# Performance work log

Hardware: AMD Instinct MI355X
Metric: run time of the kernel (lower is better)

Reference implementation:

```python
import jax, jax.numpy as jnp
import numpy as np

B, S, D, H = 2, 2048, 1024, 16
DK = D // H


def setup_inputs() -> dict:
    key = jax.random.key(0)
    ks = jax.random.split(key, 13)
    scale = 1.0 / np.sqrt(D)
    return {
        "query": jax.random.normal(ks[0], (B, S, D), jnp.float32),
        "key": jax.random.normal(ks[1], (B, S, D), jnp.float32),
        "value": jax.random.normal(ks[2], (B, S, D), jnp.float32),
        "mask": jax.random.randint(ks[3], (B, S, S), 0, 2, jnp.int32),
        "Wq": jax.random.normal(ks[4], (D, D), jnp.float32) * scale,
        "bq": jnp.zeros((D,), jnp.float32),
        "Wk": jax.random.normal(ks[5], (D, D), jnp.float32) * scale,
        "bk": jnp.zeros((D,), jnp.float32),
        "Wv": jax.random.normal(ks[6], (D, D), jnp.float32) * scale,
        "bv": jnp.zeros((D,), jnp.float32),
        "Wo": jax.random.normal(ks[7], (D, D), jnp.float32) * scale,
        "bo": jnp.zeros((D,), jnp.float32),
    }


def _split_heads(x):
    # [B,S,D] -> [B,H,S,DK]
    b, s, _ = x.shape
    return x.reshape(b, s, H, DK).transpose(0, 2, 1, 3)


def reference(query, key, value, mask, Wq, bq, Wk, bk, Wv, bv, Wo, bo):
    q = _split_heads(query @ Wq + bq)
    k = _split_heads(key @ Wk + bk)
    v = _split_heads(value @ Wv + bv)
    # scaled dot-product scores [B,H,Sq,Sk]
    scores = jnp.einsum("bhqd,bhkd->bhqk", q, k) / jnp.sqrt(jnp.float32(DK))
    scores = jnp.where(mask[:, None, :, :] == 0, jnp.float32(-1e9), scores)
    p_attn = jax.nn.softmax(scores, axis=-1)  # dropout p=0.0 -> identity
    x = jnp.einsum("bhqk,bhkd->bhqd", p_attn, v)
    x = x.transpose(0, 2, 1, 3).reshape(query.shape[0], -1, D)
    return x @ Wo + bo
```

## Files before the change

### kernel.cpp

```cpp
#include <hip/hip_runtime.h>
#include <cstdint>

#define B_ 2
#define S_ 2048
#define D_ 1024
#define H_ 16
#define DK_ 64
#define SCALE_ 0.18033688011112042f

typedef float f32x4 __attribute__((ext_vector_type(4)));
typedef float f32x16 __attribute__((ext_vector_type(16)));
typedef __bf16 bf16x8 __attribute__((ext_vector_type(8)));
typedef unsigned short u16x8 __attribute__((ext_vector_type(8)));
typedef unsigned short u16x4 __attribute__((ext_vector_type(4)));
typedef unsigned int u32x4 __attribute__((ext_vector_type(4)));

__device__ __forceinline__ unsigned short f2bf(float x) {
  unsigned int u = __builtin_bit_cast(unsigned int, x);
  u += 0x7FFFu + ((u >> 16) & 1u);
  return (unsigned short)(u >> 16);
}

__device__ __forceinline__ void gload16(const void* g, void* l) {
  __builtin_amdgcn_global_load_lds((__attribute__((address_space(1))) void*)(void*)g,
                                   (__attribute__((address_space(3))) void*)l, 16, 0, 0);
}

__device__ __forceinline__ float exp2v(float x) {
  float r;
  asm("v_exp_f32 %0, %1" : "=v"(r) : "v"(x));
  return r;
}

__device__ __forceinline__ unsigned int cvtpk(float a, float b) {
  unsigned int r;
  asm("v_cvt_pk_bf16_f32 %0, %1, %2" : "=v"(r) : "v"(a), "v"(b));
  return r;
}

__device__ __forceinline__ unsigned int bit_mask(unsigned int w, int bit) {
#if __has_builtin(__builtin_amdgcn_sbfe)
  return (unsigned int)__builtin_amdgcn_sbfe((int)w, bit, 1);
#else
  return (unsigned int)((int)(w << (31 - bit)) >> 31);
#endif
}

__global__ __launch_bounds__(256) void prep_kernel(
    const float* __restrict__ q, const float* __restrict__ k, const float* __restrict__ v,
    unsigned short* __restrict__ oq, unsigned short* __restrict__ ok,
    unsigned short* __restrict__ ov,
    const float* __restrict__ w0, const float* __restrict__ w1,
    const float* __restrict__ w2, const float* __restrict__ w3,
    unsigned short* o0, unsigned short* o1, unsigned short* o2, unsigned short* o3,
    const int* __restrict__ mask, unsigned int* __restrict__ mb) {
  __shared__ float t[32][33];
  const int bid = blockIdx.x;
  const int tid = threadIdx.x;
  if (bid < 6144) {
    const int z = bid >> 11, vb = bid & 2047;
    const float* in = z == 0 ? q : z == 1 ? k : v;
    unsigned short* out = z == 0 ? oq : z == 1 ? ok : ov;
    const int n = B_ * S_ * D_;
    int idx = vb * 256 + tid;
#pragma unroll
    for (int i = idx * 4; i < n; i += 2048 * 256 * 4) {
      f32x4 vv = *(const f32x4*)(in + i);
      u16x4 o;
#pragma unroll
      for (int j = 0; j < 4; ++j) o[j] = f2bf(vv[j]);
      *(u16x4*)(out + i) = o;
    }
  } else if (bid < 10240) {
    const int r = bid - 6144;
    const int z = r >> 10, rr = r & 1023;
    const float* W;
    unsigned short* O;
    float sc = 1.f;
    if (z == 0) { W = w0; O = o0; sc = SCALE_; }
    else if (z == 1) { W = w1; O = o1; }
    else if (z == 2) { W = w2; O = o2; }
    else { W = w3; O = o3; }
    const int n0 = (rr & 31) * 32, k0 = (rr >> 5) * 32;
    const int tx = tid & 31, ty = tid >> 5;
    for (int i = ty; i < 32; i += 8) t[i][tx] = W[(size_t)(k0 + i) * D_ + n0 + tx];
    __syncthreads();
    for (int i = ty; i < 32; i += 8) O[(size_t)(n0 + i) * D_ + k0 + tx] = f2bf(t[tx][i] * sc);
  } else {
    const int wid = ((bid - 10240) << 2) + (tid >> 6);
    const int lane = tid & 63;
    size_t base = (size_t)wid << 6;
    unsigned long long bits = __ballot(mask[base + lane] != 0);
    if (lane == 0) *(unsigned long long*)(mb + (base >> 5)) = bits;
  }
}

template <int MODE, int TN, int NWN>
__device__ __forceinline__ void gemm_t(const unsigned short* __restrict__ A,
                                       const unsigned short* __restrict__ BT,
                                       const float* __restrict__ bias, float bsc,
                                       void* __restrict__ Cp, int M, int N, int K) {
  constexpr int NWM = 4 / NWN;
  constexpr int WM = 128 / NWM;
  constexpr int WN = TN / NWN;
  constexpr int MR = WM / 16, NR = WN / 16;
  __shared__ unsigned short Al[2][128 * 32];
  __shared__ unsigned short Bl[2][TN * 32];
  const int tid = threadIdx.x;
  const int lane = tid & 63;
  const int w = tid >> 6;
  const int wr = w / NWN, wc = w % NWN;
  const int nwg = gridDim.x * gridDim.y;
  const int wg = blockIdx.x + gridDim.x * blockIdx.y;
  const int work = (wg & 7) * (nwg >> 3) + (wg >> 3);
  const int nx = N / TN;
  const int m0 = (work / nx) * 128, n0 = (work % nx) * TN;

  f32x4 acc[MR][NR] = {};
  const int nk = K / 32;
  const int srow = lane >> 2;
  const int scol = ((lane & 3) ^ ((lane >> 3) & 3)) * 8;

  const int fr = lane & 15;
  const int rsw = ((lane >> 4) ^ ((fr >> 1) & 3)) * 8;

  auto stage = [&](int kt, int bufi) {
#pragma unroll
    for (int it = 0; it < 2; ++it) {
      int chunk = it * 4 + w;
      gload16(A + (size_t)(m0 + chunk * 16 + srow) * K + kt * 32 + scol,
              &Al[bufi][chunk * 512]);
    }
#pragma unroll
    for (int it = 0; it < TN / 64; ++it) {
      int chunk = it * 4 + w;
      gload16(BT + (size_t)(n0 + chunk * 16 + srow) * K + kt * 32 + scol,
              &Bl[bufi][chunk * 512]);
    }
  };

  stage(0, 0);
  for (int kt = 0; kt < nk; ++kt) {
    const int buf = kt & 1;
    __syncthreads();
    if (kt + 1 < nk) stage(kt + 1, buf ^ 1);
    bf16x8 af[MR], bf[NR];
#pragma unroll
    for (int i = 0; i < MR; ++i)
      af[i] = __builtin_bit_cast(bf16x8,
          *(const u16x8*)&Al[buf][(wr * WM + i * 16 + fr) * 32 + rsw]);
#pragma unroll
    for (int j = 0; j < NR; ++j)
      bf[j] = __builtin_bit_cast(bf16x8,
          *(const u16x8*)&Bl[buf][(wc * WN + j * 16 + fr) * 32 + rsw]);
    __builtin_amdgcn_s_setprio(1);
#pragma unroll
    for (int i = 0; i < MR; ++i)
#pragma unroll
      for (int j = 0; j < NR; ++j)
        acc[i][j] = __builtin_amdgcn_mfma_f32_16x16x32_bf16(af[i], bf[j], acc[i][j], 0, 0, 0);
    __builtin_amdgcn_s_setprio(0);
  }

  const int rg = (lane >> 4) * 4;
  const int cg = lane & 15;
#pragma unroll
  for (int i = 0; i < MR; ++i)
#pragma unroll
    for (int j = 0; j < NR; ++j) {
      int col = n0 + wc * WN + j * 16 + cg;
      float bv = bias[col] * bsc;
#pragma unroll
      for (int e = 0; e < 4; ++e) {
        int row = m0 + wr * WM + i * 16 + rg + e;
        float v = acc[i][j][e] + bv;
        if (MODE == 1)
          ((float*)Cp)[(size_t)row * N + col] = v;
        else if (MODE == 0)
          ((unsigned short*)Cp)[(size_t)row * N + col] = f2bf(v);
        else
          ((unsigned short*)Cp)[((size_t)(row >> 11) * D_ + col) * S_ + (row & (S_ - 1))] = f2bf(v);
      }
    }
}

__global__ __launch_bounds__(256) void qkv_gemm_kernel(
    const unsigned short* __restrict__ xq, const unsigned short* __restrict__ xk,
    const unsigned short* __restrict__ xv, const unsigned short* __restrict__ wtq,
    const unsigned short* __restrict__ wtk, const unsigned short* __restrict__ wtv,
    const float* __restrict__ bq, const float* __restrict__ bk, const float* __restrict__ bv,
    unsigned short* q, unsigned short* k, unsigned short* vt) {
  if (blockIdx.z == 0)
    gemm_t<0, 128, 2>(xq, wtq, bq, SCALE_, (void*)q, B_ * S_, D_, D_);
  else if (blockIdx.z == 1)
    gemm_t<0, 128, 2>(xk, wtk, bk, 1.f, (void*)k, B_ * S_, D_, D_);
  else
    gemm_t<2, 128, 2>(xv, wtv, bv, 1.f, (void*)vt, B_ * S_, D_, D_);
}

__global__ __launch_bounds__(256) void out_gemm_kernel(const unsigned short* __restrict__ x,
                                                       const unsigned short* __restrict__ wto,
                                                       const float* __restrict__ bo,
                                                       float* __restrict__ out) {
  gemm_t<1, 64, 1>(x, wto, bo, 1.f, (void*)out, B_ * S_, D_, D_);
}

__global__ __launch_bounds__(256, 2) void attn_kernel(const unsigned short* __restrict__ Q,
                                                      const unsigned short* __restrict__ K,
                                                      const unsigned short* __restrict__ Vt,
                                                      const unsigned int* __restrict__ mb,
                                                      unsigned short* __restrict__ X) {
  __shared__ unsigned short Kl[2][128 * 64];
  __shared__ unsigned short Vl[2][2][64 * 64];

  const int tid = threadIdx.x;
  const int lane = tid & 63;
  const int w = tid >> 6;
  const int ql = lane & 31;
  const int hi = lane >> 5;

  const int wg = blockIdx.x + gridDim.x * blockIdx.y;
  const int swz = (wg & 7) * 64 + (wg >> 3);
  const int qt = swz & 15;
  const int bh = swz >> 4;
  const int b = bh >> 4, h = bh & 15;
  const int q_g = qt * 128 + w * 32 + ql;

  const size_t qkbase = ((size_t)b * S_) * D_ + h * DK_;
  const size_t vtbase = ((size_t)b * D_ + h * DK_) * S_;

  bf16x8 qf[4];
  {
    const unsigned short* qp = Q + qkbase + (size_t)q_g * D_ + hi * 8;
#pragma unroll
    for (int c = 0; c < 4; ++c)
      qf[c] = __builtin_bit_cast(bf16x8, *(const u16x8*)(qp + c * 16));
  }

  const int lr = lane >> 3;
  const int seg = (lane & 7) ^ lr;
  const unsigned short* Ks = K + qkbase + (size_t)(w * 32 + lr) * D_ + seg * 8;
  const unsigned short* Vs = Vt + vtbase + (size_t)(w * 16 + lr) * S_ + seg * 8;

  auto stage = [&](int kt, int bufi) {
#pragma unroll
    for (int c = 0; c < 4; ++c)
      gload16(Ks + ((size_t)kt * 128 + c * 8) * D_, &Kl[bufi][(w * 32 + c * 8) * 64]);
#pragma unroll
    for (int c = 0; c < 4; ++c)
      gload16(Vs + (size_t)((c & 1) * 8) * S_ + kt * 128 + (c >> 1) * 64,
              &Vl[bufi][c >> 1][(w * 16 + (c & 1) * 8) * 64]);
  };

  const unsigned long long* mrow =
      (const unsigned long long*)mb + ((size_t)b * S_ + q_g) * 32;

  f32x16 o0 = {}, o1 = {};
  f32x16 o2 = {};
  const int sw = (ql & 7) << 4;

  const unsigned int one2 = 0x3F803F80u;
  const bf16x8 onesf = __builtin_bit_cast(bf16x8, u32x4{one2, one2, one2, one2});

  stage(0, 0);
  const int NT = S_ / 128;

  for (int kt = 0; kt < NT; ++kt) {
    const int buf = kt & 1;
    __syncthreads();
    unsigned long long M0 = mrow[kt * 2], M1 = mrow[kt * 2 + 1];

    bf16x8 kf[2][2][4];
#pragma unroll
    for (int hh = 0; hh < 2; ++hh) {
      const char* Kb = (const char*)&Kl[buf][hh * 64 * 64];
#pragma unroll
      for (int r = 0; r < 2; ++r)
#pragma unroll
        for (int c = 0; c < 4; ++c)
          kf[hh][r][c] = __builtin_bit_cast(
              bf16x8, *(const u16x8*)(Kb + (((r * 32 + ql) * 128 + c * 32 + hi * 16) ^ sw)));
    }
    if (kt < NT - 1) stage(kt + 1, buf ^ 1);

    f32x16 s[2][2] = {};
    __builtin_amdgcn_s_setprio(1);
#pragma unroll
    for (int hh = 0; hh < 2; ++hh)
#pragma unroll
      for (int c = 0; c < 4; ++c) {
        s[hh][0] = __builtin_amdgcn_mfma_f32_32x32x16_bf16(kf[hh][0][c], qf[c], s[hh][0], 0, 0, 0);
        s[hh][1] = __builtin_amdgcn_mfma_f32_32x32x16_bf16(kf[hh][1][c], qf[c], s[hh][1], 0, 0, 0);
      }
    __builtin_amdgcn_s_setprio(0);

    bf16x8 vf[2][2][4];
#pragma unroll
    for (int hh = 0; hh < 2; ++hh) {
      const char* Vb = (const char*)&Vl[buf][hh][0];
#pragma unroll
      for (int nt = 0; nt < 2; ++nt)
#pragma unroll
        for (int kc = 0; kc < 4; ++kc)
          vf[hh][nt][kc] = __builtin_bit_cast(
              bf16x8, *(const u16x8*)(Vb + (((nt * 32 + ql) * 128 + kc * 32 + hi * 16) ^ sw)));
    }

    u32x4 pw[2][4];
#pragma unroll
    for (int hh = 0; hh < 2; ++hh) {
      const unsigned long long M = hh ? M1 : M0;
      unsigned int W0 = (unsigned int)(M >> (hi * 4));
      unsigned int W1 = (unsigned int)(M >> (32 + hi * 4));
#pragma unroll
      for (int r = 0; r < 16; ++r) {
        const int krl = (r & 3) + 8 * (r >> 2);
        unsigned int mk0 = bit_mask(W0, krl);
        float p0 = exp2v(s[hh][0][r]);
        s[hh][0][r] = __builtin_bit_cast(float, __builtin_bit_cast(unsigned int, p0) & mk0);
        unsigned int mk1 = bit_mask(W1, krl);
        float p1 = exp2v(s[hh][1][r]);
        s[hh][1][r] = __builtin_bit_cast(float, __builtin_bit_cast(unsigned int, p1) & mk1);
      }
#pragma unroll
      for (int kc = 0; kc < 4; ++kc) {
        const int rb = (kc & 1) * 8;
        const int st = kc >> 1;
        unsigned int w0 = cvtpk(s[hh][st][rb + 0], s[hh][st][rb + 1]);
        unsigned int w1 = cvtpk(s[hh][st][rb + 2], s[hh][st][rb + 3]);
        unsigned int w2 = cvtpk(s[hh][st][rb + 4], s[hh][st][rb + 5]);
        unsigned int w3 = cvtpk(s[hh][st][rb + 6], s[hh][st][rb + 7]);
        unsigned int u0, u1, u2, u3;
#if __has_builtin(__builtin_amdgcn_permlane32_swap)
        { auto r02 = __builtin_amdgcn_permlane32_swap(w0, w2, false, false);
          u0 = r02[0]; u2 = r02[1]; }
        { auto r13 = __builtin_amdgcn_permlane32_swap(w1, w3, false, false);
          u1 = r13[0]; u3 = r13[1]; }
#else
        { unsigned int t0 = (unsigned int)__shfl_xor((int)w0, 32);
          unsigned int t2 = (unsigned int)__shfl_xor((int)w2, 32);
          u0 = hi ? t2 : w0; u2 = hi ? w2 : t0;
          unsigned int t1 = (unsigned int)__shfl_xor((int)w1, 32);
          unsigned int t3 = (unsigned int)__shfl_xor((int)w3, 32);
          u1 = hi ? t3 : w1; u3 = hi ? w3 : t1; }
#endif
        pw[hh][kc] = u32x4{u0, u1, u2, u3};
      }
    }

    __builtin_amdgcn_s_setprio(1);
#pragma unroll
    for (int hh = 0; hh < 2; ++hh)
#pragma unroll
      for (int kc = 0; kc < 4; ++kc) {
        bf16x8 pf = __builtin_bit_cast(bf16x8, pw[hh][kc]);
        o0 = __builtin_amdgcn_mfma_f32_32x32x16_bf16(vf[hh][0][kc], pf, o0, 0, 0, 0);
        o1 = __builtin_amdgcn_mfma_f32_32x32x16_bf16(vf[hh][1][kc], pf, o1, 0, 0, 0);
        o2 = __builtin_amdgcn_mfma_f32_32x32x16_bf16(onesf, pf, o2, 0, 0, 0);
      }
    __builtin_amdgcn_s_setprio(0);
  }

  float inv = 1.f / o2[0];
  unsigned short* Xp = X + ((size_t)b * S_ + q_g) * D_ + h * DK_;
#pragma unroll
  for (int rb = 0; rb < 4; ++rb) {
    int d0 = 8 * rb + 4 * hi;
    *(unsigned int*)(Xp + d0) = cvtpk(o0[4 * rb + 0] * inv, o0[4 * rb + 1] * inv);
    *(unsigned int*)(Xp + d0 + 2) = cvtpk(o0[4 * rb + 2] * inv, o0[4 * rb + 3] * inv);
    *(unsigned int*)(Xp + 32 + d0) = cvtpk(o1[4 * rb + 0] * inv, o1[4 * rb + 1] * inv);
    *(unsigned int*)(Xp + 32 + d0 + 2) = cvtpk(o1[4 * rb + 2] * inv, o1[4 * rb + 3] * inv);
  }
}

extern "C" void kernel_launch(void* const* d_in, const int* in_sizes, int n_in,
                              void* d_out, int out_size, void* d_ws, size_t ws_size,
                              hipStream_t stream) {
  const float* query = (const float*)d_in[0];
  const float* key = (const float*)d_in[1];
  const float* value = (const float*)d_in[2];
  const int* mask = (const int*)d_in[3];
  const float* Wq = (const float*)d_in[4];
  const float* bq = (const float*)d_in[5];
  const float* Wk = (const float*)d_in[6];
  const float* bk = (const float*)d_in[7];
  const float* Wv = (const float*)d_in[8];
  const float* bv = (const float*)d_in[9];
  const float* Wo = (const float*)d_in[10];
  const float* bo = (const float*)d_in[11];
  float* out = (float*)d_out;

  const size_t ACT = (size_t)B_ * S_ * D_;
  const size_t WSZ = (size_t)D_ * D_;
  unsigned short* ws = (unsigned short*)d_ws;
  unsigned short* xq = ws;
  unsigned short* xk = xq + ACT;
  unsigned short* xv = xk + ACT;
  unsigned short* wtq = xv + ACT;
  unsigned short* wtk = wtq + WSZ;
  unsigned short* wtv = wtk + WSZ;
  unsigned short* wto = wtv + WSZ;
  unsigned short* qb = wto + WSZ;
  unsigned short* kb = qb + ACT;
  unsigned short* vt = kb + ACT;
  unsigned int* mbp = (unsigned int*)(vt + ACT);
  unsigned short* xb = xq;

  prep_kernel<<<43008, 256, 0, stream>>>(query, key, value, xq, xk, xv,
                                         Wq, Wk, Wv, Wo, wtq, wtk, wtv, wto,
                                         mask, mbp);

  dim3 gg(8, 32, 3);
  qkv_gemm_kernel<<<gg, 256, 0, stream>>>(xq, xk, xv, wtq, wtk, wtv, bq, bk, bv, qb, kb, vt);

  dim3 ag(S_ / 128, B_ * H_);
  attn_kernel<<<ag, 256, 0, stream>>>(qb, kb, vt, mbp, xb);

  dim3 og(16, 32, 1);
  out_gemm_kernel<<<og, 256, 0, stream>>>(xb, wto, bo, out);
}
```

Measured before the change: 153.7 us.

## Software-pipeline attention halves so QK MFMA overlaps previous half's softmax and PV

Splits each 128-key tile into two 64-key halves. The QK^T MFMAs of one half are now interleaved with the exp/mask/pack and PV MFMAs of the previous half, carrying the second half across loop iterations. The aim is to hide the VALU softmax work behind matrix-core work. In exchange it keeps more live registers (two score sets and two V fragment sets), which may lower occupancy or cause spills.

Result: no change. 155.3 us (+1.0%).

```diff
diff --git a/kernel.cpp b/kernel.cpp
--- a/kernel.cpp
+++ b/kernel.cpp
@@ -262,104 +262,124 @@
   const unsigned int one2 = 0x3F803F80u;
   const bf16x8 onesf = __builtin_bit_cast(bf16x8, u32x4{one2, one2, one2, one2});
 
+  f32x16 sA[2], sB[2];
+  bf16x8 vfA[2][4], vfB[2][4];
+  unsigned long long M_A = 0, M_B = 0;
+
+  auto smPV = [&](f32x16 (&S)[2], unsigned long long M, bf16x8 (&V)[2][4]) {
+    unsigned int W0 = (unsigned int)(M >> (hi * 4));
+    unsigned int W1 = (unsigned int)(M >> (32 + hi * 4));
+#pragma unroll
+    for (int r = 0; r < 16; ++r) {
+      const int krl = (r & 3) + 8 * (r >> 2);
+      unsigned int mk0 = bit_mask(W0, krl);
+      float p0 = exp2v(S[0][r]);
+      S[0][r] = __builtin_bit_cast(float, __builtin_bit_cast(unsigned int, p0) & mk0);
+      unsigned int mk1 = bit_mask(W1, krl);
+      float p1 = exp2v(S[1][r]);
+      S[1][r] = __builtin_bit_cast(float, __builtin_bit_cast(unsigned int, p1) & mk1);
+    }
+    u32x4 pw[4];
+#pragma unroll
+    for (int kc = 0; kc < 4; ++kc) {
+      const int rb = (kc & 1) * 8;
+      const int st = kc >> 1;
+      unsigned int w0 = cvtpk(S[st][rb + 0], S[st][rb + 1]);
+      unsigned int w1 = cvtpk(S[st][rb + 2], S[st][rb + 3]);
+      unsigned int w2 = cvtpk(S[st][rb + 4], S[st][rb + 5]);
+      unsigned int w3 = cvtpk(S[st][rb + 6], S[st][rb + 7]);
+      unsigned int u0, u1, u2, u3;
+#if __has_builtin(__builtin_amdgcn_permlane32_swap)
+      { auto r02 = __builtin_amdgcn_permlane32_swap(w0, w2, false, false);
+        u0 = r02[0]; u2 = r02[1]; }
+      { auto r13 = __builtin_amdgcn_permlane32_swap(w1, w3, false, false);
+        u1 = r13[0]; u3 = r13[1]; }
+#else
+      { unsigned int t0 = (unsigned int)__shfl_xor((int)w0, 32);
+        unsigned int t2 = (unsigned int)__shfl_xor((int)w2, 32);
+        u0 = hi ? t2 : w0; u2 = hi ? w2 : t0;
+        unsigned int t1 = (unsigned int)__shfl_xor((int)w1, 32);
+        unsigned int t3 = (unsigned int)__shfl_xor((int)w3, 32);
+        u1 = hi ? t3 : w1; u3 = hi ? w3 : t1; }
+#endif
+      pw[kc] = u32x4{u0, u1, u2, u3};
+    }
+    __builtin_amdgcn_s_setprio(1);
+#pragma unroll
+    for (int kc = 0; kc < 4; ++kc) {
+      bf16x8 pf = __builtin_bit_cast(bf16x8, pw[kc]);
+      o0 = __builtin_amdgcn_mfma_f32_32x32x16_bf16(V[0][kc], pf, o0, 0, 0, 0);
+      o1 = __builtin_amdgcn_mfma_f32_32x32x16_bf16(V[1][kc], pf, o1, 0, 0, 0);
+      o2 = __builtin_amdgcn_mfma_f32_32x32x16_bf16(onesf, pf, o2, 0, 0, 0);
+    }
+    __builtin_amdgcn_s_setprio(0);
+  };
+
   stage(0, 0);
   const int NT = S_ / 128;
 
   for (int kt = 0; kt < NT; ++kt) {
     const int buf = kt & 1;
     __syncthreads();
-    unsigned long long M0 = mrow[kt * 2], M1 = mrow[kt * 2 + 1];
-
-    bf16x8 kf[2][2][4];
-#pragma unroll
-    for (int hh = 0; hh < 2; ++hh) {
-      const char* Kb = (const char*)&Kl[buf][hh * 64 * 64];
+
+    {
+      const char* Kb = (const char*)&Kl[buf][0];
+      const char* Vb = (const char*)&Vl[buf][0][0];
+      bf16x8 kf[2][4];
 #pragma unroll
       for (int r = 0; r < 2; ++r)
 #pragma unroll
         for (int c = 0; c < 4; ++c)
-          kf[hh][r][c] = __builtin_bit_cast(
+          kf[r][c] = __builtin_bit_cast(
               bf16x8, *(const u16x8*)(Kb + (((r * 32 + ql) * 128 + c * 32 + hi * 16) ^ sw)));
-    }
-    if (kt < NT - 1) stage(kt + 1, buf ^ 1);
-
-    f32x16 s[2][2] = {};
-    __builtin_amdgcn_s_setprio(1);
-#pragma unroll
-    for (int hh = 0; hh < 2; ++hh)
+#pragma unroll
+      for (int nt = 0; nt < 2; ++nt)
+#pragma unroll
+        for (int kc = 0; kc < 4; ++kc)
+          vfA[nt][kc] = __builtin_bit_cast(
+              bf16x8, *(const u16x8*)(Vb + (((nt * 32 + ql) * 128 + kc * 32 + hi * 16) ^ sw)));
+      if (kt < NT - 1) stage(kt + 1, buf ^ 1);
+      M_A = mrow[kt * 2];
+      sA[0] = (f32x16){}; sA[1] = (f32x16){};
+      __builtin_amdgcn_s_setprio(1);
 #pragma unroll
       for (int c = 0; c < 4; ++c) {
-        s[hh][0] = __builtin_amdgcn_mfma_f32_32x32x16_bf16(kf[hh][0][c], qf[c], s[hh][0], 0, 0, 0);
-        s[hh][1] = __builtin_amdgcn_mfma_f32_32x32x16_bf16(kf[hh][1][c], qf[c], s[hh][1], 0, 0, 0);
+        sA[0] = __builtin_amdgcn_mfma_f32_32x32x16_bf16(kf[0][c], qf[c], sA[0], 0, 0, 0);
+        sA[1] = __builtin_amdgcn_mfma_f32_32x32x16_bf16(kf[1][c], qf[c], sA[1], 0, 0, 0);
       }
-    __builtin_amdgcn_s_setprio(0);
-
-    bf16x8 vf[2][2][4];
-#pragma unroll
-    for (int hh = 0; hh < 2; ++hh) {
-      const char* Vb = (const char*)&Vl[buf][hh][0];
+      __builtin_amdgcn_s_setprio(0);
+      if (kt != 0) smPV(sB, M_B, vfB);
+    }
+
+    {
+      const char* Kb = (const char*)&Kl[buf][64 * 64];
+      const char* Vb = (const char*)&Vl[buf][1][0];
+      bf16x8 kf[2][4];
+#pragma unroll
+      for (int r = 0; r < 2; ++r)
+#pragma unroll
+        for (int c = 0; c < 4; ++c)
+          kf[r][c] = __builtin_bit_cast(
+              bf16x8, *(const u16x8*)(Kb + (((r * 32 + ql) * 128 + c * 32 + hi * 16) ^ sw)));
 #pragma unroll
       for (int nt = 0; nt < 2; ++nt)
 #pragma unroll
         for (int kc = 0; kc < 4; ++kc)
-          vf[hh][nt][kc] = __builtin_bit_cast(
+          vfB[nt][kc] = __builtin_bit_cast(
               bf16x8, *(const u16x8*)(Vb + (((nt * 32 + ql) * 128 + kc * 32 + hi * 16) ^ sw)));
-    }
-
-    u32x4 pw[2][4];
-#pragma unroll
-    for (int hh = 0; hh < 2; ++hh) {
-      const unsigned long long M = hh ? M1 : M0;
-      unsigned int W0 = (unsigned int)(M >> (hi * 4));
-      unsigned int W1 = (unsigned int)(M >> (32 + hi * 4));
-#pragma unroll
-      for (int r = 0; r < 16; ++r) {
-        const int krl = (r & 3) + 8 * (r >> 2);
-        unsigned int mk0 = bit_mask(W0, krl);
-        float p0 = exp2v(s[hh][0][r]);
-        s[hh][0][r] = __builtin_bit_cast(float, __builtin_bit_cast(unsigned int, p0) & mk0);
-        unsigned int mk1 = bit_mask(W1, krl);
-        float p1 = exp2v(s[hh][1][r]);
-        s[hh][1][r] = __builtin_bit_cast(float, __builtin_bit_cast(unsigned int, p1) & mk1);
+      M_B = mrow[kt * 2 + 1];
+      sB[0] = (f32x16){}; sB[1] = (f32x16){};
+      __builtin_amdgcn_s_setprio(1);
+#pragma unroll
+      for (int c = 0; c < 4; ++c) {
+        sB[0] = __builtin_amdgcn_mfma_f32_32x32x16_bf16(kf[0][c], qf[c], sB[0], 0, 0, 0);
+        sB[1] = __builtin_amdgcn_mfma_f32_32x32x16_bf16(kf[1][c], qf[c], sB[1], 0, 0, 0);
       }
-#pragma unroll
-      for (int kc = 0; kc < 4; ++kc) {
-        const int rb = (kc & 1) * 8;
-        const int st = kc >> 1;
-        unsigned int w0 = cvtpk(s[hh][st][rb + 0], s[hh][st][rb + 1]);
-        unsigned int w1 = cvtpk(s[hh][st][rb + 2], s[hh][st][rb + 3]);
-        unsigned int w2 = cvtpk(s[hh][st][rb + 4], s[hh][st][rb + 5]);
-        unsigned int w3 = cvtpk(s[hh][st][rb + 6], s[hh][st][rb + 7]);
-        unsigned int u0, u1, u2, u3;
-#if __has_builtin(__builtin_amdgcn_permlane32_swap)
-        { auto r02 = __builtin_amdgcn_permlane32_swap(w0, w2, false, false);
-          u0 = r02[0]; u2 = r02[1]; }
-        { auto r13 = __builtin_amdgcn_permlane32_swap(w1, w3, false, false);
-          u1 = r13[0]; u3 = r13[1]; }
-#else
-        { unsigned int t0 = (unsigned int)__shfl_xor((int)w0, 32);
-          unsigned int t2 = (unsigned int)__shfl_xor((int)w2, 32);
-          u0 = hi ? t2 : w0; u2 = hi ? w2 : t0;
-          unsigned int t1 = (unsigned int)__shfl_xor((int)w1, 32);
-          unsigned int t3 = (unsigned int)__shfl_xor((int)w3, 32);
-          u1 = hi ? t3 : w1; u3 = hi ? w3 : t1; }
-#endif
-        pw[hh][kc] = u32x4{u0, u1, u2, u3};
-      }
-    }
-
-    __builtin_amdgcn_s_setprio(1);
-#pragma unroll
-    for (int hh = 0; hh < 2; ++hh)
-#pragma unroll
-      for (int kc = 0; kc < 4; ++kc) {
-        bf16x8 pf = __builtin_bit_cast(bf16x8, pw[hh][kc]);
-        o0 = __builtin_amdgcn_mfma_f32_32x32x16_bf16(vf[hh][0][kc], pf, o0, 0, 0, 0);
-        o1 = __builtin_amdgcn_mfma_f32_32x32x16_bf16(vf[hh][1][kc], pf, o1, 0, 0, 0);
-        o2 = __builtin_amdgcn_mfma_f32_32x32x16_bf16(onesf, pf, o2, 0, 0, 0);
-      }
-    __builtin_amdgcn_s_setprio(0);
+      __builtin_amdgcn_s_setprio(0);
+      smPV(sA, M_A, vfA);
+    }
   }
+  smPV(sB, M_B, vfB);
 
   float inv = 1.f / o2[0];
   unsigned short* Xp = X + ((size_t)b * S_ + q_g) * D_ + h * DK_;
```
